# Kernel optimization log

Hardware: AMD Instinct MI355X
Metric: run time of the kernel (lower is better)

Reference implementation:

```python
import jax, jax.numpy as jnp
import numpy as np

N = 16384   # points (batch=1, divisible by patch_size so padding is identity)
C = 512     # channels
H = 8       # num_heads
K = 1024    # patch_size
G = 48      # voxel grid extent
EPS = 1e-5
SCALE = (C // H) ** -0.5


def setup_inputs() -> dict:
    rng = np.random.default_rng(0)
    # unique occupied voxels
    flat = rng.choice(G ** 3, size=N, replace=False)
    gx = flat // (G * G); gy = (flat // G) % G; gz = flat % G
    coords = np.stack([gx, gy, gz], 1).astype(np.int64)
    # occupancy LUT on padded grid -> neighbor index per 3x3x3 kernel offset (-1 = empty)
    lut = -np.ones(((G + 2) ** 3,), np.int64)
    def flt(c):
        return ((c[:, 0] + 1) * (G + 2) + (c[:, 1] + 1)) * (G + 2) + (c[:, 2] + 1)
    lut[flt(coords)] = np.arange(N)
    offs = np.array([[dx, dy, dz] for dx in (-1, 0, 1) for dy in (-1, 0, 1) for dz in (-1, 0, 1)], np.int64)
    nbr = np.stack([lut[flt(coords + o)] for o in offs], 1)  # [N,27]
    # Morton (z-order) serialization order
    def spread(v):
        v = v.astype(np.int64); r = np.zeros_like(v)
        for b in range(6):
            r |= ((v >> b) & 1) << (3 * b)
        return r
    code = (spread(gx) << 2) | (spread(gy) << 1) | spread(gz)
    order = np.argsort(code, kind='stable').astype(np.int32)

    key = jax.random.key(0)
    ks = jax.random.split(key, 8)
    s = 0.02
    p = lambda k, shape: jax.random.normal(k, shape, jnp.float32) * s
    return dict(
        feat=jax.random.normal(ks[0], (N, C), jnp.float32),
        neighbor_idx=jnp.asarray(nbr, jnp.int32),
        order=jnp.asarray(order, jnp.int32),
        cpe_w=p(ks[1], (27, C, C)), cpe_b=jnp.zeros((C,), jnp.float32),
        cpe_lin_w=p(ks[2], (C, C)), cpe_lin_b=jnp.zeros((C,), jnp.float32),
        cpe_ln_g=jnp.ones((C,), jnp.float32), cpe_ln_b=jnp.zeros((C,), jnp.float32),
        ln1_g=jnp.ones((C,), jnp.float32), ln1_b=jnp.zeros((C,), jnp.float32),
        qkv_w=p(ks[3], (3 * C, C)), qkv_b=jnp.zeros((3 * C,), jnp.float32),
        proj_w=p(ks[4], (C, C)), proj_b=jnp.zeros((C,), jnp.float32),
        ln2_g=jnp.ones((C,), jnp.float32), ln2_b=jnp.zeros((C,), jnp.float32),
        fc1_w=p(ks[5], (4 * C, C)), fc1_b=jnp.zeros((4 * C,), jnp.float32),
        fc2_w=p(ks[6], (C, 4 * C)), fc2_b=jnp.zeros((C,), jnp.float32),
    )


def _ln(x, g, b):
    m = x.mean(-1, keepdims=True)
    v = ((x - m) ** 2).mean(-1, keepdims=True)
    return (x - m) * jax.lax.rsqrt(v + EPS) * g + b


def _block(feat, neighbor_idx, order, cpe_w, cpe_b, cpe_lin_w, cpe_lin_b,
           cpe_ln_g, cpe_ln_b, ln1_g, ln1_b, qkv_w, qkv_b, proj_w, proj_b,
           ln2_g, ln2_b, fc1_w, fc1_b, fc2_w, fc2_b):
    # ---- CPE: SubMConv3d(3x3x3) -> Linear -> LayerNorm, residual ----
    valid = neighbor_idx >= 0
    idx = jnp.maximum(neighbor_idx, 0)
    h = jnp.zeros_like(feat)
    for kk in range(27):  # fixed kernel volume
        g = jnp.where(valid[:, kk:kk + 1], feat[idx[:, kk]], 0.0)
        h = h + g @ cpe_w[kk].T
    h = h + cpe_b
    h = h @ cpe_lin_w.T + cpe_lin_b
    h = _ln(h, cpe_ln_g, cpe_ln_b)
    feat = feat + h
    # ---- Serialized windowed attention (pre-norm, residual) ----
    x = _ln(feat, ln1_g, ln1_b)
    qkv = (x @ qkv_w.T + qkv_b)[order]                 # gather by serialized order
    qkv = qkv.reshape(N // K, K, 3, H, C // H)         # [P,K,3,H,hd]
    q = qkv[:, :, 0].transpose(0, 2, 1, 3)             # [P,H,K,hd]
    k = qkv[:, :, 1].transpose(0, 2, 1, 3)
    v = qkv[:, :, 2].transpose(0, 2, 1, 3)
    attn = jax.nn.softmax(jnp.einsum('phkd,phjd->phkj', q * SCALE, k), axis=-1)
    o = jnp.einsum('phkj,phjd->phkd', attn, v).transpose(0, 2, 1, 3).reshape(N, C)
    inverse = jnp.argsort(order)                       # scatter back
    o = o[inverse] @ proj_w.T + proj_b
    feat = feat + o
    # ---- MLP (pre-norm, residual) ----
    x = _ln(feat, ln2_g, ln2_b)
    x = jax.nn.gelu(x @ fc1_w.T + fc1_b, approximate=False)
    x = x @ fc2_w.T + fc2_b
    return feat + x


def reference(feat, neighbor_idx, order, cpe_w, cpe_b, cpe_lin_w, cpe_lin_b,
              cpe_ln_g, cpe_ln_b, ln1_g, ln1_b, qkv_w, qkv_b, proj_w, proj_b,
              ln2_g, ln2_b, fc1_w, fc1_b, fc2_w, fc2_b):
    return _block(feat, neighbor_idx, order, cpe_w, cpe_b, cpe_lin_w, cpe_lin_b,
                  cpe_ln_g, cpe_ln_b, ln1_g, ln1_b, qkv_w, qkv_b, proj_w, proj_b,
                  ln2_g, ln2_b, fc1_w, fc1_b, fc2_w, fc2_b)
```

## Files before the change

### kernel.cpp

```cpp
#include <hip/hip_runtime.h>
#include <math.h>

typedef unsigned short u16;
typedef unsigned int u32;
typedef unsigned long long u64;
typedef __attribute__((ext_vector_type(8))) short short8;
typedef __attribute__((ext_vector_type(4))) float f32x4;

#define NPTS 16384
#define MAXP 98304
#define MAXTILE 768

__device__ __forceinline__ u16 f2bf(float f) {
  u32 u = __float_as_uint(f);
  u = (u + 0x7fffu + ((u >> 16) & 1u)) >> 16;
  return (u16)u;
}
__device__ __forceinline__ float bf2f(u16 u) {
  return __uint_as_float((u32)u << 16);
}

__device__ __forceinline__ void gl2lds16(const u16* g, u16* l) {
  __builtin_amdgcn_global_load_lds(
      (const __attribute__((address_space(1))) u32*)g,
      (__attribute__((address_space(3))) u32*)l, 16, 0, 0);
}

__device__ __forceinline__ float wredsum(float v) {
#pragma unroll
  for (int m = 1; m < 64; m <<= 1) v += __shfl_xor(v, m, 64);
  return v;
}

__global__ void cvt_comb(const float* __restrict__ feat,
                         const float* __restrict__ w0, const float* __restrict__ w1,
                         const float* __restrict__ w2, const float* __restrict__ w3,
                         const float* __restrict__ w4, const float* __restrict__ w5,
                         u16* __restrict__ dst) {
  const int i = blockIdx.x * 256 + threadIdx.x;
  if (i >= 4718720) return;
  ushort4 o;
  if (i < 2097280) {
    if (i < 2097152) {
      float4 v = ((const float4*)feat)[i];
      o.x = f2bf(v.x); o.y = f2bf(v.y); o.z = f2bf(v.z); o.w = f2bf(v.w);
    } else {
      o.x = 0; o.y = 0; o.z = 0; o.w = 0;
    }
  } else {
    const int j = i - 2097280;
    const float* s;
    int li;
    if (j < 1769472) { s = w0; li = j; }
    else if (j < 1835008) { s = w1; li = j - 1769472; }
    else if (j < 2031616) { s = w2; li = j - 1835008; }
    else if (j < 2097152) { s = w3; li = j - 2031616; }
    else if (j < 2359296) { s = w4; li = j - 2097152; }
    else { s = w5; li = j - 2359296; }
    float4 v = ((const float4*)s)[li];
    o.x = f2bf(v.x); o.y = f2bf(v.y); o.z = f2bf(v.z); o.w = f2bf(v.w);
  }
  ((ushort4*)dst)[i] = o;
}

__global__ void mkinv(const int* __restrict__ order, int* __restrict__ inv) {
  int i = blockIdx.x * 256 + threadIdx.x;
  if (i < NPTS) inv[order[i]] = i;
}

__global__ __launch_bounds__(256) void cpe_cnt(const int* __restrict__ nbr,
                                               int* __restrict__ wcnt) {
  const int wglob = blockIdx.x * 4 + (threadIdx.x >> 6);
  const int lane = threadIdx.x & 63;
  const int i = wglob * 64 + lane;
  const int* row = nbr + i * 27;
#pragma unroll 1
  for (int kk = 0; kk < 27; kk++) {
    const u64 m = __ballot(row[kk] >= 0);
    if (lane == 0) wcnt[wglob * 27 + kk] = (int)__popcll(m);
  }
}

__global__ __launch_bounds__(256) void cpe_plan(
    const int* __restrict__ wcnt, int* __restrict__ chunkoff,
    int* __restrict__ off, int* __restrict__ tkk, int* __restrict__ meta,
    int* __restrict__ pairj) {
  __shared__ int s_cnt[27], s_off[27], s_ts[27], s_tk[27];
  const int tid = threadIdx.x;
  if (tid < 27) {
    int run = 0;
#pragma unroll 1
    for (int c = 0; c < 256; c++) {
      chunkoff[c * 27 + tid] = run;
      run += wcnt[c * 27 + tid];
    }
    s_cnt[tid] = run;
  }
  __syncthreads();
  if (tid == 0) {
    int pos = 0, t = 0;
#pragma unroll 1
    for (int kk = 0; kk < 27; kk++) {
      s_off[kk] = pos;
      off[kk] = pos;
      int tk = (s_cnt[kk] + 127) >> 7;
      if (pos + tk * 128 > MAXP) tk = (MAXP - pos) >> 7;
      s_ts[kk] = t;
      s_tk[kk] = tk;
      t += tk;
      pos += tk * 128;
    }
    meta[0] = t;
  }
  __syncthreads();
#pragma unroll 1
  for (int kk = 0; kk < 27; kk++) {
    const int ts = s_ts[kk], tk = s_tk[kk];
    for (int u = tid; u < tk; u += 256) tkk[ts + u] = kk;
    const int base = s_off[kk], total = s_cnt[kk], padded = tk * 128;
    for (int p2 = total + tid; p2 < padded; p2 += 256) pairj[base + p2] = NPTS;
  }
}

__global__ __launch_bounds__(256) void cpe_scat(
    const int* __restrict__ nbr, const int* __restrict__ chunkoff,
    const int* __restrict__ off, int* __restrict__ pairj,
    int* __restrict__ pairpos) {
  const int wglob = blockIdx.x * 4 + (threadIdx.x >> 6);
  const int lane = threadIdx.x & 63;
  const int i = wglob * 64 + lane;
  const int* row = nbr + i * 27;
  const u64 below = (1ull << lane) - 1ull;
#pragma unroll 1
  for (int kk = 0; kk < 27; kk++) {
    const int v = row[kk];
    const bool valid = v >= 0;
    const u64 m = __ballot(valid);
    int pp = -1;
    if (valid) {
      const int t = off[kk] + chunkoff[wglob * 27 + kk] + (int)__popcll(m & below);
      if (t < MAXP) { pairj[t] = v; pp = t; }
    }
    pairpos[i * 27 + kk] = pp;
  }
}

__global__ __launch_bounds__(256, 2) void gemm_pair(
    const u16* __restrict__ Abase, const u16* __restrict__ Bw,
    const int* __restrict__ meta, const int* __restrict__ tkk,
    const int* __restrict__ pairj, u16* __restrict__ outp) {
  if ((int)blockIdx.y >= meta[0]) return;
  __shared__ __align__(16) u16 sA[128 * 32];
  __shared__ __align__(16) u16 sB[128 * 32];
  const int tid = threadIdx.x;
  const int wave = tid >> 6, lane = tid & 63;
  const int quad = lane >> 4, tl = lane & 15;
  const int wr = wave >> 1, wc = wave & 1;
  const int p0 = blockIdx.y * 128, n0 = blockIdx.x * 128;
  const int kk = tkk[blockIdx.y];
  const int srow = lane >> 2, scol = lane & 3;

  int r[2]; int ca[2];
#pragma unroll
  for (int o = 0; o < 2; o++) {
    r[o] = wave * 32 + o * 16 + srow;
    const int sw = (r[o] + (r[o] >> 2)) & 3;
    ca[o] = (scol ^ sw) * 8;
  }
  const int j0 = pairj[p0 + r[0]];
  const int j1 = pairj[p0 + r[1]];
  const u16* a0 = Abase + (size_t)j0 * 512 + ca[0];
  const u16* a1 = Abase + (size_t)j1 * 512 + ca[1];
  const u16* b0 = Bw + (size_t)kk * 262144 + (size_t)(n0 + r[0]) * 512 + ca[0];
  const u16* b1 = Bw + (size_t)kk * 262144 + (size_t)(n0 + r[1]) * 512 + ca[1];
  u16* ldsA0 = &sA[(wave * 32) * 32];
  u16* ldsA1 = &sA[(wave * 32 + 16) * 32];
  u16* ldsB0 = &sB[(wave * 32) * 32];
  u16* ldsB1 = &sB[(wave * 32 + 16) * 32];

  f32x4 acc[4][4] = {};
#pragma unroll 1
  for (int kc = 0; kc < 512; kc += 32) {
    __syncthreads();
    gl2lds16(a0 + kc, ldsA0);
    gl2lds16(b0 + kc, ldsB0);
    gl2lds16(a1 + kc, ldsA1);
    gl2lds16(b1 + kc, ldsB1);
    __syncthreads();
    short8 fa[4], fb[4];
#pragma unroll
    for (int i = 0; i < 4; i++) {
      const int ra = wr * 64 + i * 16 + tl;
      fa[i] = *(const short8*)&sA[ra * 32 + ((quad ^ ((ra + (ra >> 2)) & 3)) * 8)];
      const int rb = wc * 64 + i * 16 + tl;
      fb[i] = *(const short8*)&sB[rb * 32 + ((quad ^ ((rb + (rb >> 2)) & 3)) * 8)];
    }
#pragma unroll
    for (int i = 0; i < 4; i++)
#pragma unroll
      for (int j = 0; j < 4; j++)
        acc[i][j] = __builtin_amdgcn_mfma_f32_16x16x32_bf16(fa[i], fb[j], acc[i][j], 0, 0, 0);
  }

#pragma unroll
  for (int i = 0; i < 4; i++) {
    const int pB = p0 + wr * 64 + i * 16 + quad * 4;
#pragma unroll
    for (int j = 0; j < 4; j++) {
      const int n = n0 + wc * 64 + j * 16 + tl;
      f32x4 c = acc[i][j];
#pragma unroll
      for (int rr = 0; rr < 4; rr++)
        outp[(size_t)(pB + rr) * 512 + n] = f2bf(c[rr]);
    }
  }
}

__global__ __launch_bounds__(256, 4) void cpe_reduce(
    const u16* __restrict__ outp, const int* __restrict__ pairpos,
    const float* __restrict__ bias, u16* __restrict__ h) {
  const int wave = threadIdx.x >> 6, lane = threadIdx.x & 63;
  const int i = blockIdx.x * 4 + wave;
  const int c = lane * 8;
  float acc[8];
  const float4 b0 = *(const float4*)(bias + c);
  const float4 b1 = *(const float4*)(bias + c + 4);
  acc[0] = b0.x; acc[1] = b0.y; acc[2] = b0.z; acc[3] = b0.w;
  acc[4] = b1.x; acc[5] = b1.y; acc[6] = b1.z; acc[7] = b1.w;
  const int* pp = pairpos + i * 27;
#pragma unroll 1
  for (int kk = 0; kk < 27; kk++) {
    const int pos = pp[kk];
    if (pos >= 0) {
      const u16* row = outp + (size_t)pos * 512 + c;
      ushort4 u0 = *(const ushort4*)row;
      ushort4 u1 = *(const ushort4*)(row + 4);
      acc[0] += bf2f(u0.x); acc[1] += bf2f(u0.y);
      acc[2] += bf2f(u0.z); acc[3] += bf2f(u0.w);
      acc[4] += bf2f(u1.x); acc[5] += bf2f(u1.y);
      acc[6] += bf2f(u1.z); acc[7] += bf2f(u1.w);
    }
  }
  ushort4 o0, o1;
  o0.x = f2bf(acc[0]); o0.y = f2bf(acc[1]); o0.z = f2bf(acc[2]); o0.w = f2bf(acc[3]);
  o1.x = f2bf(acc[4]); o1.y = f2bf(acc[5]); o1.z = f2bf(acc[6]); o1.w = f2bf(acc[7]);
  *(ushort4*)(h + (size_t)i * 512 + c) = o0;
  *(ushort4*)(h + (size_t)i * 512 + c + 4) = o1;
}

__global__ __launch_bounds__(256) void vtrans(const u16* __restrict__ vr,
                                              u16* __restrict__ vt) {
  __shared__ u16 t[64 * 72];
  const int bid = blockIdx.x;
  const int ph = bid >> 4, jt = bid & 15;
  const u16* src = vr + (size_t)ph * 65536 + jt * 64 * 64;
  u16* dst = vt + (size_t)ph * 65536 + jt * 64;
  const int tid = threadIdx.x;
  {
    const int j = tid >> 2, d0 = (tid & 3) * 16;
    uint4 w0 = *(const uint4*)(src + j * 64 + d0);
    uint4 w1 = *(const uint4*)(src + j * 64 + d0 + 8);
    *(uint4*)&t[j * 72 + d0] = w0;
    *(uint4*)&t[j * 72 + d0 + 8] = w1;
  }
  __syncthreads();
  {
    const int dr = tid >> 2, j0 = (tid & 3) * 16;
    u16 tmp[16];
#pragma unroll
    for (int e = 0; e < 16; e++) tmp[e] = t[(j0 + e) * 72 + dr];
    *(uint4*)(dst + (size_t)dr * 1024 + j0) = *(uint4*)&tmp[0];
    *(uint4*)(dst + (size_t)dr * 1024 + j0 + 8) = *(uint4*)&tmp[8];
  }
}

enum { EP_BF16 = 0, EP_QKV = 2, EP_RES = 3, EP_GELU = 4 };

template <int EP>
__global__ __launch_bounds__(256, 2) void gemm_nt(
    const u16* __restrict__ A, const u16* __restrict__ B, int M, int N, int K,
    const float* __restrict__ bias, float* __restrict__ outf,
    u16* __restrict__ outb, const float* __restrict__ res,
    const int* __restrict__ inv, u16* __restrict__ oq, u16* __restrict__ okk,
    u16* __restrict__ ov) {
  __shared__ __align__(16) u16 sA[128 * 32];
  __shared__ __align__(16) u16 sB[128 * 32];
  const int tid = threadIdx.x;
  const int wave = tid >> 6, lane = tid & 63;
  const int quad = lane >> 4, tl = lane & 15;
  const int wr = wave >> 1, wc = wave & 1;
  const int m0 = blockIdx.x * 128, n0 = blockIdx.y * 128;
  const int srow = lane >> 2, scol = lane & 3;

  f32x4 acc[4][4] = {};

  for (int kt = 0; kt < K; kt += 32) {
    __syncthreads();
#pragma unroll
    for (int o = 0; o < 2; o++) {
      const int r = wave * 32 + o * 16 + srow;
      const int sw = (r + (r >> 2)) & 3;
      const int ca = (scol ^ sw) * 8;
      gl2lds16(A + (size_t)(m0 + r) * K + kt + ca, &sA[(wave * 32 + o * 16) * 32]);
      gl2lds16(B + (size_t)(n0 + r) * K + kt + ca, &sB[(wave * 32 + o * 16) * 32]);
    }
    __syncthreads();
    short8 fa[4], fb[4];
#pragma unroll
    for (int i = 0; i < 4; i++) {
      const int ra = wr * 64 + i * 16 + tl;
      fa[i] = *(const short8*)&sA[ra * 32 + ((quad ^ ((ra + (ra >> 2)) & 3)) * 8)];
      const int rb = wc * 64 + i * 16 + tl;
      fb[i] = *(const short8*)&sB[rb * 32 + ((quad ^ ((rb + (rb >> 2)) & 3)) * 8)];
    }
#pragma unroll
    for (int i = 0; i < 4; i++)
#pragma unroll
      for (int j = 0; j < 4; j++)
        acc[i][j] = __builtin_amdgcn_mfma_f32_16x16x32_bf16(fa[i], fb[j], acc[i][j], 0, 0, 0);
  }

#pragma unroll
  for (int i = 0; i < 4; i++) {
    const int mB = m0 + wr * 64 + i * 16 + quad * 4;
#pragma unroll
    for (int j = 0; j < 4; j++) {
      const int n = n0 + wc * 64 + j * 16 + tl;
      const float bv = bias[n];
      f32x4 c = acc[i][j];
#pragma unroll
      for (int r = 0; r < 4; r++) {
        const int m = mB + r;
        float v = c[r] + bv;
        if (EP == EP_BF16) {
          outb[(size_t)m * N + n] = f2bf(v);
        } else if (EP == EP_RES) {
          outf[(size_t)m * N + n] = v + res[(size_t)m * N + n];
        } else if (EP == EP_GELU) {
          float g = 0.5f * v * (1.0f + erff(v * 0.70710678118654752f));
          outb[(size_t)m * N + n] = f2bf(g);
        } else if (EP == EP_QKV) {
          const int s = n >> 9, hh = (n >> 6) & 7, d = n & 63;
          const int pos = inv[m];
          const size_t base = (size_t)((pos >> 10) * 8 + hh) * 65536;
          const int jj = pos & 1023;
          if (s == 0) oq[base + (size_t)jj * 64 + d] = f2bf(v * 0.125f);
          else if (s == 1) okk[base + (size_t)jj * 64 + d] = f2bf(v);
          else ov[base + (size_t)jj * 64 + d] = f2bf(v);
        }
      }
    }
  }
}

__global__ __launch_bounds__(256, 2) void gemm_fc2(
    const u16* __restrict__ A, const u16* __restrict__ B, u16* __restrict__ part) {
  __shared__ __align__(16) u16 sA[128 * 32];
  __shared__ __align__(16) u16 sB[128 * 32];
  const int tid = threadIdx.x;
  const int wave = tid >> 6, lane = tid & 63;
  const int quad = lane >> 4, tl = lane & 15;
  const int wr = wave >> 1, wc = wave & 1;
  const int m0 = blockIdx.x * 128, n0 = blockIdx.y * 128;
  const int kb = blockIdx.z * 1024;
  const int srow = lane >> 2, scol = lane & 3;

  f32x4 acc[4][4] = {};
  for (int kt = kb; kt < kb + 1024; kt += 32) {
    __syncthreads();
#pragma unroll
    for (int o = 0; o < 2; o++) {
      const int r = wave * 32 + o * 16 + srow;
      const int sw = (r + (r >> 2)) & 3;
      const int ca = (scol ^ sw) * 8;
      gl2lds16(A + (size_t)(m0 + r) * 2048 + kt + ca, &sA[(wave * 32 + o * 16) * 32]);
      gl2lds16(B + (size_t)(n0 + r) * 2048 + kt + ca, &sB[(wave * 32 + o * 16) * 32]);
    }
    __syncthreads();
    short8 fa[4], fb[4];
#pragma unroll
    for (int i = 0; i < 4; i++) {
      const int ra = wr * 64 + i * 16 + tl;
      fa[i] = *(const short8*)&sA[ra * 32 + ((quad ^ ((ra + (ra >> 2)) & 3)) * 8)];
      const int rb = wc * 64 + i * 16 + tl;
      fb[i] = *(const short8*)&sB[rb * 32 + ((quad ^ ((rb + (rb >> 2)) & 3)) * 8)];
    }
#pragma unroll
    for (int i = 0; i < 4; i++)
#pragma unroll
      for (int j = 0; j < 4; j++)
        acc[i][j] = __builtin_amdgcn_mfma_f32_16x16x32_bf16(fa[i], fb[j], acc[i][j], 0, 0, 0);
  }
  u16* pz = part + (size_t)blockIdx.z * NPTS * 512;
#pragma unroll
  for (int i = 0; i < 4; i++) {
    const int mB = m0 + wr * 64 + i * 16 + quad * 4;
#pragma unroll
    for (int j = 0; j < 4; j++) {
      const int n = n0 + wc * 64 + j * 16 + tl;
      f32x4 c = acc[i][j];
#pragma unroll
      for (int rr = 0; rr < 4; rr++)
        pz[(size_t)(mB + rr) * 512 + n] = f2bf(c[rr]);
    }
  }
}

__global__ void fc2_red(const u16* __restrict__ part, const float* __restrict__ bias,
                        float* __restrict__ out) {
  const int i = blockIdx.x * 256 + threadIdx.x;
  const ushort4 a = ((const ushort4*)part)[i];
  const ushort4 b = ((const ushort4*)part)[i + 2097152];
  const float4 bb = ((const float4*)bias)[i & 127];
  float4 o = ((const float4*)out)[i];
  o.x += bf2f(a.x) + bf2f(b.x) + bb.x;
  o.y += bf2f(a.y) + bf2f(b.y) + bb.y;
  o.z += bf2f(a.z) + bf2f(b.z) + bb.z;
  o.w += bf2f(a.w) + bf2f(b.w) + bb.w;
  ((float4*)out)[i] = o;
}

__global__ __launch_bounds__(256, 2) void attn(
    const u16* __restrict__ qs, const u16* __restrict__ kk_s,
    const u16* __restrict__ vts, const int* __restrict__ order,
    u16* __restrict__ obf) {
  __shared__ __align__(16) u16 Qt[128 * 64];
  __shared__ __align__(16) u16 Kt[64 * 64];
  __shared__ __align__(16) u16 Vt[64 * 64];
  __shared__ __align__(16) u16 Pl[4][32 * 72];
  const int tid = threadIdx.x;
  const int wave = tid >> 6, lane = tid & 63;
  const int quad = lane >> 4, tl = lane & 15;
  const int bid = blockIdx.x;
  const int p = bid >> 6, h = (bid >> 3) & 7, qt = bid & 7;
  const size_t base = (size_t)(p * 8 + h) * 65536;

  {
    const u16* Qg = qs + base + qt * 8192;
#pragma unroll
    for (int i = 0; i < 4; i++) {
      const int op = wave * 4 + i;
      const int r = op * 8 + (lane >> 3);
      const int c8 = ((lane & 7) ^ (r & 7)) * 8;
      gl2lds16(Qg + r * 64 + c8, &Qt[op * 512]);
    }
  }

  float ls[2][4] = {};
  f32x4 acco[2][4] = {};

  for (int kt = 0; kt < 16; kt++) {
    __syncthreads();
    const u16* Kg = kk_s + base + kt * 4096;
    const u16* Vg = vts + base + kt * 64;
#pragma unroll
    for (int i = 0; i < 2; i++) {
      const int op = wave * 2 + i;
      const int r = op * 8 + (lane >> 3);
      const int c8 = ((lane & 7) ^ (r & 7)) * 8;
      gl2lds16(Kg + r * 64 + c8, &Kt[op * 512]);
      gl2lds16(Vg + r * 1024 + c8, &Vt[op * 512]);
    }
    __syncthreads();

    f32x4 accs[2][4] = {};
#pragma unroll
    for (int kd = 0; kd < 2; kd++) {
      short8 qa[2], kb[4];
#pragma unroll
      for (int a = 0; a < 2; a++) {
        const int r = wave * 32 + a * 16 + tl;
        const int oct = (kd * 4 + quad) ^ (r & 7);
        qa[a] = *(const short8*)&Qt[r * 64 + oct * 8];
      }
#pragma unroll
      for (int b = 0; b < 4; b++) {
        const int r = b * 16 + tl;
        const int oct = (kd * 4 + quad) ^ (r & 7);
        kb[b] = *(const short8*)&Kt[r * 64 + oct * 8];
      }
#pragma unroll
      for (int a = 0; a < 2; a++)
#pragma unroll
        for (int b = 0; b < 4; b++)
          accs[a][b] = __builtin_amdgcn_mfma_f32_16x16x32_bf16(qa[a], kb[b], accs[a][b], 0, 0, 0);
    }

    u16* plw = &Pl[wave][0];
#pragma unroll
    for (int a = 0; a < 2; a++)
#pragma unroll
      for (int c = 0; c < 4; c++) {
#pragma unroll
        for (int r = 0; r < 4; r++) {
          const float pe = __expf(accs[a][c][r]);
          accs[a][c][r] = pe;
          ls[a][r] += pe;
          plw[(a * 16 + quad * 4 + r) * 72 + c * 16 + tl] = f2bf(pe);
        }
      }

#pragma unroll
    for (int k2 = 0; k2 < 2; k2++) {
      short8 pa[2], vb[4];
#pragma unroll
      for (int a = 0; a < 2; a++)
        pa[a] = *(const short8*)&plw[(a * 16 + tl) * 72 + k2 * 32 + quad * 8];
#pragma unroll
      for (int b = 0; b < 4; b++) {
        const int rb = b * 16 + tl;
        vb[b] = *(const short8*)&Vt[rb * 64 + (((k2 * 4 + quad) ^ (rb & 7)) * 8)];
      }
#pragma unroll
      for (int a = 0; a < 2; a++)
#pragma unroll
        for (int b = 0; b < 4; b++)
          acco[a][b] = __builtin_amdgcn_mfma_f32_16x16x32_bf16(pa[a], vb[b], acco[a][b], 0, 0, 0);
    }
  }

#pragma unroll
  for (int a = 0; a < 2; a++)
#pragma unroll
    for (int r = 0; r < 4; r++) {
#pragma unroll
      for (int mk = 1; mk < 16; mk <<= 1) ls[a][r] += __shfl_xor(ls[a][r], mk, 64);
    }

  const int q0 = p * 1024 + qt * 128 + wave * 32;
#pragma unroll
  for (int a = 0; a < 2; a++)
#pragma unroll
    for (int r = 0; r < 4; r++) {
      const int orig = order[q0 + a * 16 + quad * 4 + r];
      const float il = 1.0f / ls[a][r];
#pragma unroll
      for (int b = 0; b < 4; b++)
        obf[(size_t)orig * 512 + h * 64 + b * 16 + tl] = f2bf(acco[a][b][r] * il);
    }
}

__global__ __launch_bounds__(256, 4) void ln_fuse1(
    const u16* __restrict__ h2, const float* __restrict__ feat,
    const float* __restrict__ cg, const float* __restrict__ cb,
    const float* __restrict__ g1, const float* __restrict__ b1,
    float* __restrict__ feat1, u16* __restrict__ xbf) {
  const int wave = threadIdx.x >> 6, lane = threadIdx.x & 63;
  const size_t row = (size_t)blockIdx.x * 4 + wave;
  const int c0 = lane * 4, c1 = 256 + lane * 4;
  const u16* hr = h2 + row * 512;
  ushort4 ha = *(const ushort4*)(hr + c0);
  ushort4 hb = *(const ushort4*)(hr + c1);
  float h[8];
  h[0] = bf2f(ha.x); h[1] = bf2f(ha.y); h[2] = bf2f(ha.z); h[3] = bf2f(ha.w);
  h[4] = bf2f(hb.x); h[5] = bf2f(hb.y); h[6] = bf2f(hb.z); h[7] = bf2f(hb.w);
  float s = 0.0f, q = 0.0f;
#pragma unroll
  for (int i = 0; i < 8; i++) { s += h[i]; q += h[i] * h[i]; }
  s = wredsum(s); q = wredsum(q);
  const float mean = s * (1.0f / 512.0f);
  const float var = q * (1.0f / 512.0f) - mean * mean;
  const float rs = rsqrtf(var + 1e-5f);
  float4 ga = *(const float4*)(cg + c0), gb = *(const float4*)(cg + c1);
  float4 ba = *(const float4*)(cb + c0), bb = *(const float4*)(cb + c1);
  const float* fr = feat + row * 512;
  float4 fa = *(const float4*)(fr + c0), fb = *(const float4*)(fr + c1);
  float f[8];
  f[0] = fa.x + (h[0] - mean) * rs * ga.x + ba.x;
  f[1] = fa.y + (h[1] - mean) * rs * ga.y + ba.y;
  f[2] = fa.z + (h[2] - mean) * rs * ga.z + ba.z;
  f[3] = fa.w + (h[3] - mean) * rs * ga.w + ba.w;
  f[4] = fb.x + (h[4] - mean) * rs * gb.x + bb.x;
  f[5] = fb.y + (h[5] - mean) * rs * gb.y + bb.y;
  f[6] = fb.z + (h[6] - mean) * rs * gb.z + bb.z;
  f[7] = fb.w + (h[7] - mean) * rs * gb.w + bb.w;
  float* f1r = feat1 + row * 512;
  *(float4*)(f1r + c0) = make_float4(f[0], f[1], f[2], f[3]);
  *(float4*)(f1r + c1) = make_float4(f[4], f[5], f[6], f[7]);
  float s2 = 0.0f, q2 = 0.0f;
#pragma unroll
  for (int i = 0; i < 8; i++) { s2 += f[i]; q2 += f[i] * f[i]; }
  s2 = wredsum(s2); q2 = wredsum(q2);
  const float mean2 = s2 * (1.0f / 512.0f);
  const float var2 = q2 * (1.0f / 512.0f) - mean2 * mean2;
  const float rs2 = rsqrtf(var2 + 1e-5f);
  float4 g1a = *(const float4*)(g1 + c0), g1b = *(const float4*)(g1 + c1);
  float4 b1a = *(const float4*)(b1 + c0), b1b = *(const float4*)(b1 + c1);
  ushort4 o0, o1;
  o0.x = f2bf((f[0] - mean2) * rs2 * g1a.x + b1a.x);
  o0.y = f2bf((f[1] - mean2) * rs2 * g1a.y + b1a.y);
  o0.z = f2bf((f[2] - mean2) * rs2 * g1a.z + b1a.z);
  o0.w = f2bf((f[3] - mean2) * rs2 * g1a.w + b1a.w);
  o1.x = f2bf((f[4] - mean2) * rs2 * g1b.x + b1b.x);
  o1.y = f2bf((f[5] - mean2) * rs2 * g1b.y + b1b.y);
  o1.z = f2bf((f[6] - mean2) * rs2 * g1b.z + b1b.z);
  o1.w = f2bf((f[7] - mean2) * rs2 * g1b.w + b1b.w);
  *(ushort4*)(xbf + row * 512 + c0) = o0;
  *(ushort4*)(xbf + row * 512 + c1) = o1;
}

__global__ __launch_bounds__(256, 4) void ln_only(
    const float* __restrict__ x, const float* __restrict__ g,
    const float* __restrict__ b_, u16* __restrict__ o) {
  const int wave = threadIdx.x >> 6, lane = threadIdx.x & 63;
  const size_t row = (size_t)blockIdx.x * 4 + wave;
  const int c0 = lane * 4, c1 = 256 + lane * 4;
  const float* xr = x + row * 512;
  float4 a = *(const float4*)(xr + c0);
  float4 b = *(const float4*)(xr + c1);
  float s = a.x + a.y + a.z + a.w + b.x + b.y + b.z + b.w;
  float q = a.x * a.x + a.y * a.y + a.z * a.z + a.w * a.w +
            b.x * b.x + b.y * b.y + b.z * b.z + b.w * b.w;
  s = wredsum(s); q = wredsum(q);
  const float mean = s * (1.0f / 512.0f);
  const float var = q * (1.0f / 512.0f) - mean * mean;
  const float rs = rsqrtf(var + 1e-5f);
  float4 ga = *(const float4*)(g + c0), gb = *(const float4*)(g + c1);
  float4 ba = *(const float4*)(b_ + c0), bb = *(const float4*)(b_ + c1);
  ushort4 o0, o1;
  o0.x = f2bf((a.x - mean) * rs * ga.x + ba.x);
  o0.y = f2bf((a.y - mean) * rs * ga.y + ba.y);
  o0.z = f2bf((a.z - mean) * rs * ga.z + ba.z);
  o0.w = f2bf((a.w - mean) * rs * ga.w + ba.w);
  o1.x = f2bf((b.x - mean) * rs * gb.x + bb.x);
  o1.y = f2bf((b.y - mean) * rs * gb.y + bb.y);
  o1.z = f2bf((b.z - mean) * rs * gb.z + bb.z);
  o1.w = f2bf((b.w - mean) * rs * gb.w + bb.w);
  *(ushort4*)(o + row * 512 + c0) = o0;
  *(ushort4*)(o + row * 512 + c1) = o1;
}

extern "C" void kernel_launch(void* const* d_in, const int* in_sizes, int n_in,
                              void* d_out, int out_size, void* d_ws, size_t ws_size,
                              hipStream_t stream) {
  (void)in_sizes; (void)n_in; (void)out_size; (void)ws_size;
  const float* feat = (const float*)d_in[0];
  const int* nbr = (const int*)d_in[1];
  const int* order = (const int*)d_in[2];
  const float* cpe_w = (const float*)d_in[3];
  const float* cpe_b = (const float*)d_in[4];
  const float* cpe_lin_w = (const float*)d_in[5];
  const float* cpe_lin_b = (const float*)d_in[6];
  const float* cpe_ln_g = (const float*)d_in[7];
  const float* cpe_ln_b = (const float*)d_in[8];
  const float* ln1_g = (const float*)d_in[9];
  const float* ln1_b = (const float*)d_in[10];
  const float* qkv_w = (const float*)d_in[11];
  const float* qkv_b = (const float*)d_in[12];
  const float* proj_w = (const float*)d_in[13];
  const float* proj_b = (const float*)d_in[14];
  const float* ln2_g = (const float*)d_in[15];
  const float* ln2_b = (const float*)d_in[16];
  const float* fc1_w = (const float*)d_in[17];
  const float* fc1_b = (const float*)d_in[18];
  const float* fc2_w = (const float*)d_in[19];
  const float* fc2_b = (const float*)d_in[20];
  float* out = (float*)d_out;

  char* ws = (char*)d_ws;
  size_t off = 0;
  auto alloc = [&](size_t bytes) {
    char* p = ws + off;
    off += (bytes + 255) & ~(size_t)255;
    return p;
  };
  u16* featbf = (u16*)alloc((size_t)(NPTS + 1) * 512 * 2);
  u16* w_cpe = (u16*)alloc((size_t)27 * 512 * 512 * 2);
  u16* w_cl = (u16*)alloc((size_t)512 * 512 * 2);
  u16* w_qkv = (u16*)alloc((size_t)1536 * 512 * 2);
  u16* w_proj = (u16*)alloc((size_t)512 * 512 * 2);
  u16* w_fc1 = (u16*)alloc((size_t)2048 * 512 * 2);
  u16* w_fc2 = (u16*)alloc((size_t)512 * 2048 * 2);
  u16* hbf = (u16*)alloc((size_t)NPTS * 512 * 2);
  char* big = alloc((size_t)NPTS * 2048 * 2);
  float* feat1 = (float*)alloc((size_t)NPTS * 512 * 4);
  int* inv = (int*)alloc((size_t)NPTS * 4);
  int* offs = (int*)alloc(27 * 4);
  int* meta = (int*)alloc(256);
  int* tkk = (int*)alloc((size_t)(MAXTILE + 1) * 4);
  int* pairj = (int*)alloc((size_t)MAXP * 4);
  int* pairpos = (int*)alloc((size_t)NPTS * 27 * 4);
  int* wcnt = (int*)alloc((size_t)256 * 27 * 4);
  int* chunkoff = (int*)alloc((size_t)256 * 27 * 4);

  u16* out_pair = (u16*)big;
  u16* h2 = (u16*)big;
  u16* qsb = (u16*)big;
  u16* ksb = qsb + (size_t)NPTS * 512;
  u16* vrow = ksb + (size_t)NPTS * 512;
  u16* vtb = vrow + (size_t)NPTS * 512;
  u16* tbf = (u16*)big;
  u16* fc2p = (u16*)feat1;
  u16* xbf = hbf;
  u16* obf = hbf;
  u16* x2bf = featbf;

  cvt_comb<<<dim3(18433), dim3(256), 0, stream>>>(feat, cpe_w, cpe_lin_w, qkv_w,
                                                  proj_w, fc1_w, fc2_w, featbf);
  mkinv<<<dim3(NPTS / 256), dim3(256), 0, stream>>>(order, inv);

  cpe_cnt<<<dim3(64), dim3(256), 0, stream>>>(nbr, wcnt);
  cpe_plan<<<dim3(1), dim3(256), 0, stream>>>(wcnt, chunkoff, offs, tkk, meta, pairj);
  cpe_scat<<<dim3(64), dim3(256), 0, stream>>>(nbr, chunkoff, offs, pairj, pairpos);
  gemm_pair<<<dim3(4, MAXTILE), dim3(256), 0, stream>>>(featbf, w_cpe, meta, tkk,
                                                        pairj, out_pair);
  cpe_reduce<<<dim3(NPTS / 4), dim3(256), 0, stream>>>(out_pair, pairpos, cpe_b, hbf);

  gemm_nt<EP_BF16><<<dim3(128, 4), dim3(256), 0, stream>>>(
      hbf, w_cl, NPTS, 512, 512, cpe_lin_b, nullptr, h2, nullptr, nullptr,
      nullptr, nullptr, nullptr);
  ln_fuse1<<<dim3(NPTS / 4), dim3(256), 0, stream>>>(
      h2, feat, cpe_ln_g, cpe_ln_b, ln1_g, ln1_b, feat1, xbf);
  gemm_nt<EP_QKV><<<dim3(128, 12), dim3(256), 0, stream>>>(
      xbf, w_qkv, NPTS, 1536, 512, qkv_b, nullptr, nullptr, nullptr, inv,
      qsb, ksb, vrow);
  vtrans<<<dim3(2048), dim3(256), 0, stream>>>(vrow, vtb);
  attn<<<dim3(1024), dim3(256), 0, stream>>>(qsb, ksb, vtb, order, obf);
  gemm_nt<EP_RES><<<dim3(128, 4), dim3(256), 0, stream>>>(
      obf, w_proj, NPTS, 512, 512, proj_b, out, nullptr, feat1, nullptr,
      nullptr, nullptr, nullptr);
  ln_only<<<dim3(NPTS / 4), dim3(256), 0, stream>>>(out, ln2_g, ln2_b, x2bf);
  gemm_nt<EP_GELU><<<dim3(128, 16), dim3(256), 0, stream>>>(
      x2bf, w_fc1, NPTS, 2048, 512, fc1_b, nullptr, tbf, nullptr, nullptr,
      nullptr, nullptr, nullptr);
  gemm_fc2<<<dim3(128, 4, 2), dim3(256), 0, stream>>>(tbf, w_fc2, fc2p);
  fc2_red<<<dim3(8192), dim3(256), 0, stream>>>(fc2p, fc2_b, out);
}
```

Baseline: 617.9 us.

## Remap gemm_pair and attn block order, replace split-K fc2 with fused residual GEMM

gemm_pair now runs on a 1D grid whose index groups 8 tiles by 4 column blocks, so neighbouring blocks share A rows and weight slices in cache. attn reorders block ids so the query-tile index is the slowest-varying dimension, changing which heads and patches run concurrently. The split-K fc2 GEMM and its separate bf16 partial-sum reduction kernel are replaced with a single gemm_nt EP_RES call over K=2048 that adds bias and residual in place. This removes one launch and the bf16 partial round trip, but halves fc2 parallelism to 512 blocks and relies on in-place residual reads of out being safe.

```diff
diff --git a/kernel.cpp b/kernel.cpp
--- a/kernel.cpp
+++ b/kernel.cpp
@@ -149,15 +149,18 @@
     const u16* __restrict__ Abase, const u16* __restrict__ Bw,
     const int* __restrict__ meta, const int* __restrict__ tkk,
     const int* __restrict__ pairj, u16* __restrict__ outp) {
-  if ((int)blockIdx.y >= meta[0]) return;
+  const int L = blockIdx.x;
+  const int tile = (L >> 5) * 8 + (L & 7);
+  const int n0b = (L >> 3) & 3;
+  if (tile >= meta[0]) return;
   __shared__ __align__(16) u16 sA[128 * 32];
   __shared__ __align__(16) u16 sB[128 * 32];
   const int tid = threadIdx.x;
   const int wave = tid >> 6, lane = tid & 63;
   const int quad = lane >> 4, tl = lane & 15;
   const int wr = wave >> 1, wc = wave & 1;
-  const int p0 = blockIdx.y * 128, n0 = blockIdx.x * 128;
-  const int kk = tkk[blockIdx.y];
+  const int p0 = tile * 128, n0 = n0b * 128;
+  const int kk = tkk[tile];
   const int srow = lane >> 2, scol = lane & 3;
 
   int r[2]; int ca[2];
@@ -353,73 +356,6 @@
   }
 }
 
-__global__ __launch_bounds__(256, 2) void gemm_fc2(
-    const u16* __restrict__ A, const u16* __restrict__ B, u16* __restrict__ part) {
-  __shared__ __align__(16) u16 sA[128 * 32];
-  __shared__ __align__(16) u16 sB[128 * 32];
-  const int tid = threadIdx.x;
-  const int wave = tid >> 6, lane = tid & 63;
-  const int quad = lane >> 4, tl = lane & 15;
-  const int wr = wave >> 1, wc = wave & 1;
-  const int m0 = blockIdx.x * 128, n0 = blockIdx.y * 128;
-  const int kb = blockIdx.z * 1024;
-  const int srow = lane >> 2, scol = lane & 3;
-
-  f32x4 acc[4][4] = {};
-  for (int kt = kb; kt < kb + 1024; kt += 32) {
-    __syncthreads();
-#pragma unroll
-    for (int o = 0; o < 2; o++) {
-      const int r = wave * 32 + o * 16 + srow;
-      const int sw = (r + (r >> 2)) & 3;
-      const int ca = (scol ^ sw) * 8;
-      gl2lds16(A + (size_t)(m0 + r) * 2048 + kt + ca, &sA[(wave * 32 + o * 16) * 32]);
-      gl2lds16(B + (size_t)(n0 + r) * 2048 + kt + ca, &sB[(wave * 32 + o * 16) * 32]);
-    }
-    __syncthreads();
-    short8 fa[4], fb[4];
-#pragma unroll
-    for (int i = 0; i < 4; i++) {
-      const int ra = wr * 64 + i * 16 + tl;
-      fa[i] = *(const short8*)&sA[ra * 32 + ((quad ^ ((ra + (ra >> 2)) & 3)) * 8)];
-      const int rb = wc * 64 + i * 16 + tl;
-      fb[i] = *(const short8*)&sB[rb * 32 + ((quad ^ ((rb + (rb >> 2)) & 3)) * 8)];
-    }
-#pragma unroll
-    for (int i = 0; i < 4; i++)
-#pragma unroll
-      for (int j = 0; j < 4; j++)
-        acc[i][j] = __builtin_amdgcn_mfma_f32_16x16x32_bf16(fa[i], fb[j], acc[i][j], 0, 0, 0);
-  }
-  u16* pz = part + (size_t)blockIdx.z * NPTS * 512;
-#pragma unroll
-  for (int i = 0; i < 4; i++) {
-    const int mB = m0 + wr * 64 + i * 16 + quad * 4;
-#pragma unroll
-    for (int j = 0; j < 4; j++) {
-      const int n = n0 + wc * 64 + j * 16 + tl;
-      f32x4 c = acc[i][j];
-#pragma unroll
-      for (int rr = 0; rr < 4; rr++)
-        pz[(size_t)(mB + rr) * 512 + n] = f2bf(c[rr]);
-    }
-  }
-}
-
-__global__ void fc2_red(const u16* __restrict__ part, const float* __restrict__ bias,
-                        float* __restrict__ out) {
-  const int i = blockIdx.x * 256 + threadIdx.x;
-  const ushort4 a = ((const ushort4*)part)[i];
-  const ushort4 b = ((const ushort4*)part)[i + 2097152];
-  const float4 bb = ((const float4*)bias)[i & 127];
-  float4 o = ((const float4*)out)[i];
-  o.x += bf2f(a.x) + bf2f(b.x) + bb.x;
-  o.y += bf2f(a.y) + bf2f(b.y) + bb.y;
-  o.z += bf2f(a.z) + bf2f(b.z) + bb.z;
-  o.w += bf2f(a.w) + bf2f(b.w) + bb.w;
-  ((float4*)out)[i] = o;
-}
-
 __global__ __launch_bounds__(256, 2) void attn(
     const u16* __restrict__ qs, const u16* __restrict__ kk_s,
     const u16* __restrict__ vts, const int* __restrict__ order,
@@ -432,8 +368,9 @@
   const int wave = tid >> 6, lane = tid & 63;
   const int quad = lane >> 4, tl = lane & 15;
   const int bid = blockIdx.x;
-  const int p = bid >> 6, h = (bid >> 3) & 7, qt = bid & 7;
-  const size_t base = (size_t)(p * 8 + h) * 65536;
+  const int qt = bid >> 7, ph = bid & 127;
+  const int p = ph >> 3, h = ph & 7;
+  const size_t base = (size_t)ph * 65536;
 
   {
     const u16* Qg = qs + base + qt * 8192;
@@ -690,7 +627,6 @@
   u16* vrow = ksb + (size_t)NPTS * 512;
   u16* vtb = vrow + (size_t)NPTS * 512;
   u16* tbf = (u16*)big;
-  u16* fc2p = (u16*)feat1;
   u16* xbf = hbf;
   u16* obf = hbf;
   u16* x2bf = featbf;
@@ -702,8 +638,8 @@
   cpe_cnt<<<dim3(64), dim3(256), 0, stream>>>(nbr, wcnt);
   cpe_plan<<<dim3(1), dim3(256), 0, stream>>>(wcnt, chunkoff, offs, tkk, meta, pairj);
   cpe_scat<<<dim3(64), dim3(256), 0, stream>>>(nbr, chunkoff, offs, pairj, pairpos);
-  gemm_pair<<<dim3(4, MAXTILE), dim3(256), 0, stream>>>(featbf, w_cpe, meta, tkk,
-                                                        pairj, out_pair);
+  gemm_pair<<<dim3(MAXTILE * 4), dim3(256), 0, stream>>>(featbf, w_cpe, meta, tkk,
+                                                         pairj, out_pair);
   cpe_reduce<<<dim3(NPTS / 4), dim3(256), 0, stream>>>(out_pair, pairpos, cpe_b, hbf);
 
   gemm_nt<EP_BF16><<<dim3(128, 4), dim3(256), 0, stream>>>(
@@ -723,6 +659,7 @@
   gemm_nt<EP_GELU><<<dim3(128, 16), dim3(256), 0, stream>>>(
       x2bf, w_fc1, NPTS, 2048, 512, fc1_b, nullptr, tbf, nullptr, nullptr,
       nullptr, nullptr, nullptr);
-  gemm_fc2<<<dim3(128, 4, 2), dim3(256), 0, stream>>>(tbf, w_fc2, fc2p);
-  fc2_red<<<dim3(8192), dim3(256), 0, stream>>>(fc2p, fc2_b, out);
-}
+  gemm_nt<EP_RES><<<dim3(128, 4), dim3(256), 0, stream>>>(
+      tbf, w_fc2, NPTS, 512, 2048, fc2_b, out, nullptr, out, nullptr,
+      nullptr, nullptr, nullptr);
+}
```

Result: faster. 596.2 us (-3.5%).
